# Kernel optimization log

Hardware: AMD Instinct MI355X
Metric: run time of the kernel (lower is better)

## Reference

```python
import jax, jax.numpy as jnp
import numpy as np


def setup_inputs() -> dict:
    key = jax.random.key(0)
    k1, k2 = jax.random.split(key)
    B, N, C = 16, 2049, 1024
    x = jax.random.normal(k1, (B, N, C), dtype=jnp.float32)
    # nn.Linear(dim, 3*dim, bias=False): weight applied as x @ W^T; store as (C, 3C)
    w_qkv = jax.random.normal(k2, (C, 3 * C), dtype=jnp.float32) * (1.0 / np.sqrt(C))
    return {"x": x, "w_qkv": w_qkv}


def reference(x, w_qkv):
    B, N, C = x.shape
    scale = C ** (-0.5)
    qkv = (x @ w_qkv).reshape(B, N, 3, C)  # [B,N,3,C]
    q = qkv[:, :, 0, :]  # [B,N,C]
    k = qkv[:, :, 1, :]  # [B,N,C]
    # Original computes full q @ k^T then keeps only row 0, cols 1: before softmax.
    # Mathematically identical (and efficient) to use only the CLS query row.
    q_cls = q[:, 0, :]                                   # [B,C]
    attn_cls_logits = jnp.einsum('bc,bnc->bn', q_cls, k[:, 1:, :]) * scale  # [B,N-1]
    return jax.nn.softmax(attn_cls_logits, axis=-1)
```

## Files before the change

kernel.cpp:

```cpp
#include <hip/hip_runtime.h>
#include <math.h>


#define BATCH 16
#define SEQ   2049
#define CH    1024
#define W3    3072
#define NOUT  2048
#define PD    8


__global__ __launch_bounds__(512) void qcls_part_kernel(
    const float* __restrict__ x, const float* __restrict__ w,
    float* __restrict__ part) {
    const int ci = blockIdx.x;
    const int pi = blockIdx.y;
    const int t  = threadIdx.x;
    const int lane = t & 63;
    const int wv   = t >> 6;

    __shared__ float  xs[BATCH][128];
    __shared__ float4 red[8][8][64];

    for (int i = t; i < BATCH * 128; i += 512) {
        const int b = i >> 7, dd = i & 127;
        xs[b][dd] = x[(size_t)b * SEQ * CH + pi * 128 + dd];
    }
    __syncthreads();

    const int c = ci * 256 + lane * 4;
    float4 acc[BATCH];
    #pragma unroll
    for (int b = 0; b < BATCH; ++b) acc[b] = {0.f, 0.f, 0.f, 0.f};

    const int drow0 = pi * 128 + wv * 16;
    #pragma unroll 4
    for (int dd = 0; dd < 16; ++dd) {
        const float4 wvec = *(const float4*)(w + (size_t)(drow0 + dd) * W3 + c);
        const int dl = wv * 16 + dd;
        #pragma unroll
        for (int b = 0; b < BATCH; ++b) {
            const float s = xs[b][dl];
            acc[b].x += s * wvec.x; acc[b].y += s * wvec.y;
            acc[b].z += s * wvec.z; acc[b].w += s * wvec.w;
        }
    }

    #pragma unroll
    for (int p = 0; p < 2; ++p) {
        #pragma unroll
        for (int b2 = 0; b2 < 8; ++b2)
            red[wv][b2][lane] = acc[p * 8 + b2];
        __syncthreads();
        {
            const int b = p * 8 + wv;
            float4 s = red[0][wv][lane];
            #pragma unroll
            for (int ww = 1; ww < 8; ++ww) {
                const float4 r = red[ww][wv][lane];
                s.x += r.x; s.y += r.y; s.z += r.z; s.w += r.w;
            }
            *(float4*)(part + ((size_t)pi * BATCH + b) * CH + c) = s;
        }
        __syncthreads();
    }
}

__global__ __launch_bounds__(256) void v_kernel(
    const float* __restrict__ w, const float* __restrict__ part,
    float* __restrict__ v) {
    __shared__ float qs[BATCH * CH];
    const int t = threadIdx.x;
    const float4* p4 = (const float4*)part;
    for (int i4 = t; i4 < BATCH * CH / 4; i4 += 256) {
        float4 s = p4[i4];
        #pragma unroll
        for (int p = 1; p < PD; ++p) {
            const float4 r = p4[p * (BATCH * CH / 4) + i4];
            s.x += r.x; s.y += r.y; s.z += r.z; s.w += r.w;
        }
        ((float4*)qs)[i4] = s;
    }
    __syncthreads();

    const int lane = t & 63;
    const int wave = t >> 6;
    #pragma unroll
    for (int k = 0; k < 4; ++k) {
        const int d = blockIdx.x * 16 + wave * 4 + k;
        const float* wrow = w + (size_t)d * W3 + CH;
        float4 wv4[4];
        #pragma unroll
        for (int j = 0; j < 4; ++j)
            wv4[j] = *(const float4*)(wrow + lane * 4 + j * 256);
        #pragma unroll
        for (int b = 0; b < BATCH; ++b) {
            float acc = 0.f;
            #pragma unroll
            for (int j = 0; j < 4; ++j) {
                const float4 qv = *(const float4*)(&qs[b * CH + lane * 4 + j * 256]);
                acc += wv4[j].x * qv.x + wv4[j].y * qv.y
                     + wv4[j].z * qv.z + wv4[j].w * qv.w;
            }
            #pragma unroll
            for (int off = 32; off > 0; off >>= 1)
                acc += __shfl_down(acc, off, 64);
            if (lane == 0) v[b * CH + d] = acc;
        }
    }
}

__global__ __launch_bounds__(256) void logits_kernel(
    const float* __restrict__ x, const float* __restrict__ v,
    float* __restrict__ logits) {
    const int t = threadIdx.x;
    const int lane = t & 63;
    const int row0 = blockIdx.x * 4;
    const int b = row0 >> 11;

    __shared__ float4 vs[CH / 4];
    vs[t] = ((const float4*)(v + (size_t)b * CH))[t];
    __syncthreads();

    const int row = row0 + (t >> 6);
    const int n = row & (NOUT - 1);
    const float* xrow = x + ((size_t)b * SEQ + n + 1) * CH;
    float acc = 0.f;
    #pragma unroll
    for (int j = 0; j < 4; ++j) {
        const float4 xv = *(const float4*)(xrow + lane * 4 + j * 256);
        const float4 vv = vs[lane + j * 64];
        acc += xv.x * vv.x + xv.y * vv.y + xv.z * vv.z + xv.w * vv.w;
    }
    #pragma unroll
    for (int off = 32; off > 0; off >>= 1)
        acc += __shfl_down(acc, off, 64);
    if (lane == 0) logits[row] = acc * 0.03125f;
}

__global__ __launch_bounds__(256) void softmax_kernel(
    const float* __restrict__ logits, float* __restrict__ out) {
    const int b = blockIdx.x;
    const int t = threadIdx.x;
    __shared__ float sm[256];
    float val[8];
    float m = -1e30f;
    #pragma unroll
    for (int i = 0; i < 8; ++i) {
        val[i] = logits[b * NOUT + t + i * 256];
        m = fmaxf(m, val[i]);
    }
    sm[t] = m; __syncthreads();
    for (int s = 128; s > 0; s >>= 1) {
        if (t < s) sm[t] = fmaxf(sm[t], sm[t + s]);
        __syncthreads();
    }
    const float mx = sm[0];
    __syncthreads();
    float e[8];
    float sum = 0.f;
    #pragma unroll
    for (int i = 0; i < 8; ++i) { e[i] = expf(val[i] - mx); sum += e[i]; }
    sm[t] = sum; __syncthreads();
    for (int s = 128; s > 0; s >>= 1) {
        if (t < s) sm[t] += sm[t + s];
        __syncthreads();
    }
    const float inv = 1.0f / sm[0];
    #pragma unroll
    for (int i = 0; i < 8; ++i) out[b * NOUT + t + i * 256] = e[i] * inv;
}

extern "C" void kernel_launch(void* const* d_in, const int* in_sizes, int n_in,
                              void* d_out, int out_size, void* d_ws, size_t ws_size,
                              hipStream_t stream) {
    const float* x = (const float*)d_in[0];
    const float* w = (const float*)d_in[1];
    float* out = (float*)d_out;
    float* ws = (float*)d_ws;

    float* part   = ws;
    float* vbuf   = ws + 131072;
    float* logits = ws + 147456;

    qcls_part_kernel<<<dim3(4, 8), 512, 0, stream>>>(x, w, part);
    v_kernel<<<64, 256, 0, stream>>>(w, part, vbuf);
    logits_kernel<<<8192, 256, 0, stream>>>(x, vbuf, logits);
    softmax_kernel<<<BATCH, 256, 0, stream>>>(logits, out);
}
```

Baseline: 230.4 us.

## Restructure q_cls projection to full-depth blocks and widen v_kernel grid

```diff
diff --git a/kernel.cpp b/kernel.cpp
--- a/kernel.cpp
+++ b/kernel.cpp
@@ -7,87 +7,67 @@
 #define CH    1024
 #define W3    3072
 #define NOUT  2048
-#define PD    8
+#define XSTR  1028
 
 
-__global__ __launch_bounds__(512) void qcls_part_kernel(
+__global__ __launch_bounds__(512) void qcls_kernel(
     const float* __restrict__ x, const float* __restrict__ w,
-    float* __restrict__ part) {
+    float* __restrict__ qcls) {
     const int ci = blockIdx.x;
-    const int pi = blockIdx.y;
     const int t  = threadIdx.x;
     const int lane = t & 63;
     const int wv   = t >> 6;
 
-    __shared__ float  xs[BATCH][128];
-    __shared__ float4 red[8][8][64];
+    __shared__ float  xs[BATCH * XSTR];
+    __shared__ float4 red[8][64];
 
-    for (int i = t; i < BATCH * 128; i += 512) {
-        const int b = i >> 7, dd = i & 127;
-        xs[b][dd] = x[(size_t)b * SEQ * CH + pi * 128 + dd];
+    const float4* x4 = (const float4*)x;
+    for (int i4 = t; i4 < BATCH * CH / 4; i4 += 512) {
+        const int b = i4 >> 8, d4 = i4 & 255;
+        *(float4*)(xs + b * XSTR + d4 * 4) = x4[(size_t)b * (SEQ * CH / 4) + d4];
     }
     __syncthreads();
 
-    const int c = ci * 256 + lane * 4;
-    float4 acc[BATCH];
-    #pragma unroll
-    for (int b = 0; b < BATCH; ++b) acc[b] = {0.f, 0.f, 0.f, 0.f};
+    const int b  = lane >> 2;
+    const int cc = lane & 3;
+    const int c  = ci * 16 + cc * 4;
 
-    const int drow0 = pi * 128 + wv * 16;
-    #pragma unroll 4
-    for (int dd = 0; dd < 16; ++dd) {
-        const float4 wvec = *(const float4*)(w + (size_t)(drow0 + dd) * W3 + c);
-        const int dl = wv * 16 + dd;
+    float4 acc = {0.f, 0.f, 0.f, 0.f};
+    const int d0 = wv * 128;
+    #pragma unroll 8
+    for (int dd = 0; dd < 128; ++dd) {
+        const int d = d0 + dd;
+        const float4 wvec = *(const float4*)(w + (size_t)d * W3 + c);
+        const float  s    = xs[b * XSTR + d];
+        acc.x += s * wvec.x; acc.y += s * wvec.y;
+        acc.z += s * wvec.z; acc.w += s * wvec.w;
+    }
+    red[wv][lane] = acc;
+    __syncthreads();
+
+    if (t < 64) {
+        float4 s = red[0][t];
         #pragma unroll
-        for (int b = 0; b < BATCH; ++b) {
-            const float s = xs[b][dl];
-            acc[b].x += s * wvec.x; acc[b].y += s * wvec.y;
-            acc[b].z += s * wvec.z; acc[b].w += s * wvec.w;
+        for (int ww = 1; ww < 8; ++ww) {
+            const float4 r = red[ww][t];
+            s.x += r.x; s.y += r.y; s.z += r.z; s.w += r.w;
         }
-    }
-
-    #pragma unroll
-    for (int p = 0; p < 2; ++p) {
-        #pragma unroll
-        for (int b2 = 0; b2 < 8; ++b2)
-            red[wv][b2][lane] = acc[p * 8 + b2];
-        __syncthreads();
-        {
-            const int b = p * 8 + wv;
-            float4 s = red[0][wv][lane];
-            #pragma unroll
-            for (int ww = 1; ww < 8; ++ww) {
-                const float4 r = red[ww][wv][lane];
-                s.x += r.x; s.y += r.y; s.z += r.z; s.w += r.w;
-            }
-            *(float4*)(part + ((size_t)pi * BATCH + b) * CH + c) = s;
-        }
-        __syncthreads();
+        *(float4*)(qcls + (t >> 2) * CH + ci * 16 + (t & 3) * 4) = s;
     }
 }
 
 __global__ __launch_bounds__(256) void v_kernel(
-    const float* __restrict__ w, const float* __restrict__ part,
+    const float* __restrict__ w, const float* __restrict__ qcls,
     float* __restrict__ v) {
     __shared__ float qs[BATCH * CH];
     const int t = threadIdx.x;
-    const float4* p4 = (const float4*)part;
-    for (int i4 = t; i4 < BATCH * CH / 4; i4 += 256) {
-        float4 s = p4[i4];
-        #pragma unroll
-        for (int p = 1; p < PD; ++p) {
-            const float4 r = p4[p * (BATCH * CH / 4) + i4];
-            s.x += r.x; s.y += r.y; s.z += r.z; s.w += r.w;
-        }
-        ((float4*)qs)[i4] = s;
-    }
+    for (int i = t; i < BATCH * CH; i += 256) qs[i] = qcls[i];
     __syncthreads();
-
     const int lane = t & 63;
     const int wave = t >> 6;
     #pragma unroll
-    for (int k = 0; k < 4; ++k) {
-        const int d = blockIdx.x * 16 + wave * 4 + k;
+    for (int k = 0; k < 2; ++k) {
+        const int d = blockIdx.x * 8 + wave * 2 + k;
         const float* wrow = w + (size_t)d * W3 + CH;
         float4 wv4[4];
         #pragma unroll
@@ -179,12 +159,12 @@
     float* out = (float*)d_out;
     float* ws = (float*)d_ws;
 
-    float* part   = ws;
-    float* vbuf   = ws + 131072;
-    float* logits = ws + 147456;
+    float* qcls   = ws;
+    float* vbuf   = ws + 16384;
+    float* logits = ws + 32768;
 
-    qcls_part_kernel<<<dim3(4, 8), 512, 0, stream>>>(x, w, part);
-    v_kernel<<<64, 256, 0, stream>>>(w, part, vbuf);
+    qcls_kernel<<<64, 512, 0, stream>>>(x, w, qcls);
+    v_kernel<<<128, 256, 0, stream>>>(w, qcls, vbuf);
     logits_kernel<<<8192, 256, 0, stream>>>(x, vbuf, logits);
     softmax_kernel<<<BATCH, 256, 0, stream>>>(logits, out);
 }
```

New measurement: 224.6 us. 2.5% less time.

## Split q_cls projection across more blocks with separate reduction kernel

Applied to the files above, without the earlier changes.

```diff
diff --git a/kernel.cpp b/kernel.cpp
--- a/kernel.cpp
+++ b/kernel.cpp
@@ -7,10 +7,9 @@
 #define CH    1024
 #define W3    3072
 #define NOUT  2048
-#define PD    8
 
 
-__global__ __launch_bounds__(512) void qcls_part_kernel(
+__global__ __launch_bounds__(256) void qcls_partial_kernel(
     const float* __restrict__ x, const float* __restrict__ w,
     float* __restrict__ part) {
     const int ci = blockIdx.x;
@@ -19,12 +18,12 @@
     const int lane = t & 63;
     const int wv   = t >> 6;
 
-    __shared__ float  xs[BATCH][128];
-    __shared__ float4 red[8][8][64];
+    __shared__ float  xs[BATCH][16];
+    __shared__ float4 red[4][8][64];
 
-    for (int i = t; i < BATCH * 128; i += 512) {
-        const int b = i >> 7, dd = i & 127;
-        xs[b][dd] = x[(size_t)b * SEQ * CH + pi * 128 + dd];
+    {
+        const int b = t >> 4, dd = t & 15;
+        xs[b][dd] = x[(size_t)b * SEQ * CH + pi * 16 + dd];
     }
     __syncthreads();
 
@@ -33,14 +32,16 @@
     #pragma unroll
     for (int b = 0; b < BATCH; ++b) acc[b] = {0.f, 0.f, 0.f, 0.f};
 
-    const int drow0 = pi * 128 + wv * 16;
-    #pragma unroll 4
-    for (int dd = 0; dd < 16; ++dd) {
+    const int drow0 = pi * 16 + wv * 4;
+    #pragma unroll
+    for (int dd = 0; dd < 4; ++dd) {
         const float4 wvec = *(const float4*)(w + (size_t)(drow0 + dd) * W3 + c);
-        const int dl = wv * 16 + dd;
+        const float s0 = xs[0][wv * 4 + dd];
+        acc[0].x += s0 * wvec.x; acc[0].y += s0 * wvec.y;
+        acc[0].z += s0 * wvec.z; acc[0].w += s0 * wvec.w;
         #pragma unroll
-        for (int b = 0; b < BATCH; ++b) {
-            const float s = xs[b][dl];
+        for (int b = 1; b < BATCH; ++b) {
+            const float s = xs[b][wv * 4 + dd];
             acc[b].x += s * wvec.x; acc[b].y += s * wvec.y;
             acc[b].z += s * wvec.z; acc[b].w += s * wvec.w;
         }
@@ -48,46 +49,46 @@
 
     #pragma unroll
     for (int p = 0; p < 2; ++p) {
+        __syncthreads();
         #pragma unroll
         for (int b2 = 0; b2 < 8; ++b2)
             red[wv][b2][lane] = acc[p * 8 + b2];
         __syncthreads();
-        {
-            const int b = p * 8 + wv;
-            float4 s = red[0][wv][lane];
+        #pragma unroll
+        for (int k = 0; k < 2; ++k) {
+            const int b2 = wv * 2 + k;
+            float4 s = red[0][b2][lane];
             #pragma unroll
-            for (int ww = 1; ww < 8; ++ww) {
-                const float4 r = red[ww][wv][lane];
+            for (int ww = 1; ww < 4; ++ww) {
+                const float4 r = red[ww][b2][lane];
                 s.x += r.x; s.y += r.y; s.z += r.z; s.w += r.w;
             }
-            *(float4*)(part + ((size_t)pi * BATCH + b) * CH + c) = s;
+            *(float4*)(part + ((size_t)pi * BATCH + p * 8 + b2) * CH + c) = s;
         }
-        __syncthreads();
     }
 }
 
+__global__ __launch_bounds__(256) void qcls_reduce_kernel(
+    const float* __restrict__ part, float* __restrict__ qcls) {
+    const int id = blockIdx.x * 256 + threadIdx.x;
+    float s = 0.f;
+    #pragma unroll 8
+    for (int p = 0; p < 64; ++p) s += part[(size_t)p * BATCH * CH + id];
+    qcls[id] = s;
+}
+
 __global__ __launch_bounds__(256) void v_kernel(
-    const float* __restrict__ w, const float* __restrict__ part,
+    const float* __restrict__ w, const float* __restrict__ qcls,
     float* __restrict__ v) {
     __shared__ float qs[BATCH * CH];
     const int t = threadIdx.x;
-    const float4* p4 = (const float4*)part;
-    for (int i4 = t; i4 < BATCH * CH / 4; i4 += 256) {
-        float4 s = p4[i4];
-        #pragma unroll
-        for (int p = 1; p < PD; ++p) {
-            const float4 r = p4[p * (BATCH * CH / 4) + i4];
-            s.x += r.x; s.y += r.y; s.z += r.z; s.w += r.w;
-        }
-        ((float4*)qs)[i4] = s;
-    }
+    for (int i = t; i < BATCH * CH; i += 256) qs[i] = qcls[i];
     __syncthreads();
-
     const int lane = t & 63;
     const int wave = t >> 6;
     #pragma unroll
-    for (int k = 0; k < 4; ++k) {
-        const int d = blockIdx.x * 16 + wave * 4 + k;
+    for (int k = 0; k < 2; ++k) {
+        const int d = blockIdx.x * 8 + wave * 2 + k;
         const float* wrow = w + (size_t)d * W3 + CH;
         float4 wv4[4];
         #pragma unroll
@@ -142,7 +143,10 @@
     const float* __restrict__ logits, float* __restrict__ out) {
     const int b = blockIdx.x;
     const int t = threadIdx.x;
-    __shared__ float sm[256];
+    const int lane = t & 63;
+    const int wv = t >> 6;
+    __shared__ float wred[4];
+
     float val[8];
     float m = -1e30f;
     #pragma unroll
@@ -150,23 +154,24 @@
         val[i] = logits[b * NOUT + t + i * 256];
         m = fmaxf(m, val[i]);
     }
-    sm[t] = m; __syncthreads();
-    for (int s = 128; s > 0; s >>= 1) {
-        if (t < s) sm[t] = fmaxf(sm[t], sm[t + s]);
-        __syncthreads();
-    }
-    const float mx = sm[0];
+    #pragma unroll
+    for (int off = 32; off > 0; off >>= 1)
+        m = fmaxf(m, __shfl_xor(m, off, 64));
+    if (lane == 0) wred[wv] = m;
     __syncthreads();
+    const float mx = fmaxf(fmaxf(wred[0], wred[1]), fmaxf(wred[2], wred[3]));
+    __syncthreads();
+
     float e[8];
     float sum = 0.f;
     #pragma unroll
     for (int i = 0; i < 8; ++i) { e[i] = expf(val[i] - mx); sum += e[i]; }
-    sm[t] = sum; __syncthreads();
-    for (int s = 128; s > 0; s >>= 1) {
-        if (t < s) sm[t] += sm[t + s];
-        __syncthreads();
-    }
-    const float inv = 1.0f / sm[0];
+    #pragma unroll
+    for (int off = 32; off > 0; off >>= 1)
+        sum += __shfl_xor(sum, off, 64);
+    if (lane == 0) wred[wv] = sum;
+    __syncthreads();
+    const float inv = 1.0f / (wred[0] + wred[1] + wred[2] + wred[3]);
     #pragma unroll
     for (int i = 0; i < 8; ++i) out[b * NOUT + t + i * 256] = e[i] * inv;
 }
@@ -180,11 +185,13 @@
     float* ws = (float*)d_ws;
 
     float* part   = ws;
-    float* vbuf   = ws + 131072;
-    float* logits = ws + 147456;
+    float* qcls   = ws + 1048576;
+    float* vbuf   = ws + 1048576 + 16384;
+    float* logits = ws + 1048576 + 32768;
 
-    qcls_part_kernel<<<dim3(4, 8), 512, 0, stream>>>(x, w, part);
-    v_kernel<<<64, 256, 0, stream>>>(w, part, vbuf);
+    qcls_partial_kernel<<<dim3(4, 64), 256, 0, stream>>>(x, w, part);
+    qcls_reduce_kernel<<<64, 256, 0, stream>>>(part, qcls);
+    v_kernel<<<128, 256, 0, stream>>>(w, qcls, vbuf);
     logits_kernel<<<8192, 256, 0, stream>>>(x, vbuf, logits);
     softmax_kernel<<<BATCH, 256, 0, stream>>>(logits, out);
 }
```

Result: faster. 215.7 us (-6.4%).
